# Performance work log

Measured on AMD Instinct MI355X. Metric: run time of the kernel, lower is better.

The kernel has to match this reference:

```python
import jax, jax.numpy as jnp
import numpy as np

N_A, N_B = 50000, 10000
E = 300000
IN_F, HID, BEL_OUT, INC_OUT = 256, 256, 128, 128


def _gconv(x_src, W, b, src, dst, n_src, n_dst):
    """DGL GraphConv with norm='both': D_in^{-1/2} A D_out^{-1/2} X W + b, degs clamped to >=1."""
    ones = jnp.ones(src.shape[0], x_src.dtype)
    deg_out = jnp.maximum(jax.ops.segment_sum(ones, src, num_segments=n_src), 1.0)
    deg_in = jnp.maximum(jax.ops.segment_sum(ones, dst, num_segments=n_dst), 1.0)
    h = (x_src * jax.lax.rsqrt(deg_out)[:, None]) @ W        # [n_src, out]
    agg = jax.ops.segment_sum(h[src], dst, num_segments=n_dst)  # scatter-add messages
    return agg * jax.lax.rsqrt(deg_in)[:, None] + b


def setup_inputs() -> dict:
    key = jax.random.key(0)
    ks = jax.random.split(key, 12)
    s = 1.0 / np.sqrt(IN_F)
    sh = 1.0 / np.sqrt(HID)
    return {
        "x_a": jax.random.normal(ks[0], (N_A, IN_F), jnp.float32),
        "x_b": jax.random.normal(ks[1], (N_B, IN_F), jnp.float32),
        "W1_bel": jax.random.normal(ks[2], (IN_F, HID), jnp.float32) * s,
        "b1_bel": jnp.zeros((HID,), jnp.float32),
        "W1_inc": jax.random.normal(ks[3], (IN_F, HID), jnp.float32) * s,
        "b1_inc": jnp.zeros((HID,), jnp.float32),
        "W2_bel": jax.random.normal(ks[4], (HID, BEL_OUT), jnp.float32) * sh,
        "b2_bel": jnp.zeros((BEL_OUT,), jnp.float32),
        "W2_inc": jax.random.normal(ks[5], (HID, INC_OUT), jnp.float32) * sh,
        "b2_inc": jnp.zeros((INC_OUT,), jnp.float32),
        "bel_src": jax.random.randint(ks[6], (E,), 0, N_A, jnp.int32),
        "bel_dst": jax.random.randint(ks[7], (E,), 0, N_B, jnp.int32),
        "inc_src": jax.random.randint(ks[8], (E,), 0, N_B, jnp.int32),
        "inc_dst": jax.random.randint(ks[9], (E,), 0, N_A, jnp.int32),
    }


def reference(x_a, x_b, W1_bel, b1_bel, W1_inc, b1_inc, W2_bel, b2_bel,
              W2_inc, b2_inc, bel_src, bel_dst, inc_src, inc_dst):
    n_a, n_b = x_a.shape[0], x_b.shape[0]
    # layer 1 (HeteroGraphConv, mean over a single relation per dst type = identity)
    h_b = _gconv(x_a, W1_bel, b1_bel, bel_src, bel_dst, n_a, n_b)  # 'belongs_to': A->B
    h_a = _gconv(x_b, W1_inc, b1_inc, inc_src, inc_dst, n_b, n_a)  # 'including' : B->A
    h_a = jax.nn.relu(h_a)
    h_b = jax.nn.relu(h_b)
    # layer 2
    out_b = _gconv(h_a, W2_bel, b2_bel, bel_src, bel_dst, n_a, n_b)  # [N_B, bel_out]
    out_a = _gconv(h_b, W2_inc, b2_inc, inc_src, inc_dst, n_b, n_a)  # [N_A, inc_out]
    return out_a, out_b
```

## Files before the change

### kernel.cpp

```cpp
#include <hip/hip_runtime.h>


#define NA 50000
#define NB 10000
#define NE 300000
#define GB 625
#define HB 1172
#define PB 64
#define CB 300

typedef unsigned short u16;
typedef unsigned int u32;
typedef __attribute__((ext_vector_type(8))) short short8;
typedef __attribute__((ext_vector_type(4))) float f32x4;
typedef __attribute__((ext_vector_type(2))) float f32x2;
typedef __attribute__((ext_vector_type(4))) unsigned short u16x4;

__device__ __forceinline__ float bf2f(u16 h){
  union { u32 u; float f; } x; x.u = ((u32)h) << 16; return x.f;
}
__device__ __forceinline__ u16 f2bf(float f){
  union { float f; u32 u; } x; x.f = f;
  u32 r = (x.u + 0x7FFFu + ((x.u >> 16) & 1u)) >> 16;
  return (u16)r;
}

__device__ __forceinline__ void pack_elem(int t,
    const float* __restrict__ W1b, const float* __restrict__ W1i,
    const float* __restrict__ W2b, const float* __restrict__ W2i,
    u16* __restrict__ pwh, u16* __restrict__ pwl){
  const float* W; int N; int tt;
  if (t < 65536)       { W = W1b; N = 256; tt = t; }
  else if (t < 131072) { W = W1i; N = 256; tt = t - 65536; }
  else if (t < 163840) { W = W2b; N = 128; tt = t - 131072; }
  else                 { W = W2i; N = 128; tt = t - 163840; }
  int j = tt & 7, lane = (tt >> 3) & 63, tile = tt >> 9;
  int nT = N >> 4;
  int nt = tile % nT, kt = tile / nT;
  int k = kt * 32 + ((lane >> 4) << 3) + j;
  int n = nt * 16 + (lane & 15);
  float v = W[k * N + n];
  u16 hi = f2bf(v);
  pwh[t] = hi;
  pwl[t] = f2bf(v - bf2f(hi));
}

__global__ __launch_bounds__(256) void pre_kernel(
    int* __restrict__ z, int nz, const float* __restrict__ W1i,
    u16* __restrict__ pwh, u16* __restrict__ pwl){
  int g = blockIdx.x * blockDim.x + threadIdx.x;
  int s = gridDim.x * blockDim.x;
  for (int i = g; i < nz; i += s) z[i] = 0;
  for (int t = g; t < 65536; t += s)
    pack_elem(65536 + t, nullptr, W1i, nullptr, nullptr, pwh, pwl);
}

__device__ __forceinline__ void gemm_dev(int blk, const float* __restrict__ A,
                                         const u16* __restrict__ PWH,
                                         const u16* __restrict__ PWL,
                                         const float* __restrict__ bias,
                                         const float* __restrict__ rs,
                                         float* __restrict__ Cf,
                                         u16* __restrict__ C16,
                                         int M, int nT, int wpsShift,
                                         int doRelu, int ldC, int colOff){
  int wave = blk * 4 + (threadIdx.x >> 6);
  int lane = threadIdx.x & 63;
  int strips = M >> 4;
  int strip = wave >> wpsShift;
  if (strip >= strips) return;
  int slice = wave & ((1 << wpsShift) - 1);
  int ntPer = nT >> wpsShift;
  int ntStart = slice * ntPer;
  int r16 = lane & 15, quad = lane >> 4;
  int m0 = strip << 4;
  const float* aBase = A + (size_t)(m0 + r16) * 256 + quad * 8;
  short8 ah[8], al[8];
#pragma unroll
  for (int kt = 0; kt < 8; ++kt){
    float4 p0 = *(const float4*)(aBase + kt * 32);
    float4 p1 = *(const float4*)(aBase + kt * 32 + 4);
    float v[8] = {p0.x, p0.y, p0.z, p0.w, p1.x, p1.y, p1.z, p1.w};
    short8 h, l;
#pragma unroll
    for (int j = 0; j < 8; ++j){
      u16 hb = f2bf(v[j]);
      h[j] = (short)hb;
      l[j] = (short)f2bf(v[j] - bf2f(hb));
    }
    ah[kt] = h; al[kt] = l;
  }
  float rscale[4];
#pragma unroll
  for (int r = 0; r < 4; ++r) rscale[r] = rs ? rs[m0 + quad * 4 + r] : 1.f;
  for (int nt = ntStart; nt < ntStart + ntPer; ++nt){
    f32x4 acc = {0.f, 0.f, 0.f, 0.f};
    const u16* bh = PWH + ((size_t)nt * 64 + lane) * 8;
    const u16* bl = PWL + ((size_t)nt * 64 + lane) * 8;
#pragma unroll
    for (int kt = 0; kt < 8; ++kt){
      short8 wh = *(const short8*)(bh + (size_t)kt * nT * 512);
      short8 wl = *(const short8*)(bl + (size_t)kt * nT * 512);
      acc = __builtin_amdgcn_mfma_f32_16x16x32_bf16(ah[kt], wh, acc, 0, 0, 0);
      acc = __builtin_amdgcn_mfma_f32_16x16x32_bf16(al[kt], wh, acc, 0, 0, 0);
      acc = __builtin_amdgcn_mfma_f32_16x16x32_bf16(ah[kt], wl, acc, 0, 0, 0);
    }
    int col = nt * 16 + r16;
    float bv = bias ? bias[col] : 0.f;
#pragma unroll
    for (int r = 0; r < 4; ++r){
      float v = acc[r] * rscale[r] + bv;
      if (doRelu) v = fmaxf(v, 0.f);
      size_t o = (size_t)(m0 + quad * 4 + r) * ldC + colOff + col;
      if (C16) __builtin_nontemporal_store(f2bf(v), C16 + o);
      else     __builtin_nontemporal_store(v, Cf + o);
    }
  }
}

__global__ __launch_bounds__(256) void mega_kernel(
    const float* __restrict__ xb,
    const u16* __restrict__ WH1i, const u16* __restrict__ WL1i,
    u16* __restrict__ G12,
    const int* __restrict__ bs, const int* __restrict__ bd,
    const int* __restrict__ isc, const int* __restrict__ idt,
    int* __restrict__ c_bs, int* __restrict__ c_bd,
    int* __restrict__ c_is, int* __restrict__ c_id,
    int* __restrict__ rank_bel, int* __restrict__ rank_inc,
    const float* __restrict__ W1b, const float* __restrict__ W2b,
    const float* __restrict__ W2i,
    u16* __restrict__ pwh, u16* __restrict__ pwl,
    const float* __restrict__ xa, u16* __restrict__ xa16){
  int blk = blockIdx.x;
  if (blk < GB){
    gemm_dev(blk, xb, WH1i, WL1i, nullptr, nullptr,
             nullptr, G12, NB, 16, 2, 0, 384, 0);
  } else if (blk < GB + HB){
    int g = (blk - GB) * blockDim.x + threadIdx.x;
    int s = HB * blockDim.x;
    for (int e = g; e < NE; e += s){
      atomicAdd(&c_bs[bs[e]], 1);
      rank_bel[e] = atomicAdd(&c_bd[bd[e]], 1);
      atomicAdd(&c_is[isc[e]], 1);
      rank_inc[e] = atomicAdd(&c_id[idt[e]], 1);
    }
  } else if (blk < GB + HB + PB){
    int g = (blk - GB - HB) * blockDim.x + threadIdx.x;
    int s = PB * blockDim.x;
    for (int v = g; v < 131072; v += s){
      int t = v < 65536 ? v : v + 65536;
      pack_elem(t, W1b, nullptr, W2b, W2i, pwh, pwl);
    }
  } else {
    int g = ((blk - GB - HB - PB) * blockDim.x + threadIdx.x) * 4;
    int s = CB * blockDim.x * 4;
    for (int i = g; i < NA * 256; i += s){
      float4 v = *(const float4*)(xa + i);
      u16x4 o;
      o.x = f2bf(v.x); o.y = f2bf(v.y); o.z = f2bf(v.z); o.w = f2bf(v.w);
      __builtin_nontemporal_store(o, (u16x4*)(xa16 + i));
    }
  }
}

__global__ __launch_bounds__(1024) void scan_scales_kernel(
    const int* __restrict__ c_bs, const int* __restrict__ c_bd,
    const int* __restrict__ c_is, const int* __restrict__ c_id,
    int* __restrict__ off_bel, int* __restrict__ off_inc,
    float* __restrict__ s_ob, float* __restrict__ s_ib,
    float* __restrict__ s_oi, float* __restrict__ s_ii){
  if (blockIdx.x >= 2){
    int g = (blockIdx.x - 2) * blockDim.x + threadIdx.x;
    int s = (gridDim.x - 2) * blockDim.x;
    for (int i = g; i < NA; i += s){
      int a = c_bs[i]; s_ob[i] = rsqrtf((float)(a > 1 ? a : 1));
      int b = c_id[i]; s_ii[i] = rsqrtf((float)(b > 1 ? b : 1));
      if (i < NB){
        int c = c_bd[i]; s_ib[i] = rsqrtf((float)(c > 1 ? c : 1));
        int d = c_is[i]; s_oi[i] = rsqrtf((float)(d > 1 ? d : 1));
      }
    }
    return;
  }
  const int* cnt; int* off; int n;
  if (blockIdx.x == 0){ cnt = c_bd; off = off_bel; n = NB; }
  else                { cnt = c_id; off = off_inc; n = NA; }
  __shared__ int wsum[16];
  __shared__ int carry, chunkTot;
  int tid = threadIdx.x, lane = tid & 63, wid = tid >> 6;
  if (tid == 0) carry = 0;
  __syncthreads();
  for (int base = 0; base < n; base += 4096){
    int i0 = base + tid * 4;
    int v[4];
#pragma unroll
    for (int r = 0; r < 4; ++r){ int idx = i0 + r; v[r] = (idx < n) ? cnt[idx] : 0; }
    int s = v[0] + v[1] + v[2] + v[3];
    int x = s;
#pragma unroll
    for (int d = 1; d < 64; d <<= 1){ int t = __shfl_up(x, d, 64); if (lane >= d) x += t; }
    if (lane == 63) wsum[wid] = x;
    __syncthreads();
    if (wid == 0){
      int ws = (lane < 16) ? wsum[lane] : 0;
#pragma unroll
      for (int d = 1; d < 16; d <<= 1){ int t = __shfl_up(ws, d, 64); if (lane >= d) ws += t; }
      if (lane < 16) wsum[lane] = ws;
      if (lane == 15) chunkTot = ws;
    }
    __syncthreads();
    int waveBase = (wid == 0) ? 0 : wsum[wid - 1];
    int run = carry + waveBase + (x - s);
#pragma unroll
    for (int r = 0; r < 4; ++r){ int idx = i0 + r; if (idx < n) off[idx] = run; run += v[r]; }
    __syncthreads();
    if (tid == 0) carry += chunkTot;
    __syncthreads();
  }
  if (tid == 0) off[n] = carry;
}

__global__ __launch_bounds__(256) void fill_kernel(
    const int* __restrict__ bs, const int* __restrict__ bd,
    const int* __restrict__ isc, const int* __restrict__ idt,
    const int* __restrict__ rank_bel, const int* __restrict__ rank_inc,
    const int* __restrict__ off_bel, const int* __restrict__ off_inc,
    int* __restrict__ csr_bel, int* __restrict__ csr_inc){
  int g = blockIdx.x * blockDim.x + threadIdx.x;
  int s = gridDim.x * blockDim.x;
  for (int e = g; e < NE; e += s){
    csr_bel[off_bel[bd[e]] + rank_bel[e]] = bs[e];
    csr_inc[off_inc[idt[e]] + rank_inc[e]] = isc[e];
  }
}

__global__ __launch_bounds__(256) void gemmHG_kernel(
    const float* __restrict__ Pb,
    const u16* __restrict__ WH1b, const u16* __restrict__ WL1b,
    const float* __restrict__ b1b, const float* __restrict__ s_ib,
    const u16* __restrict__ WH2i, const u16* __restrict__ WL2i,
    u16* __restrict__ G12){
  __shared__ float Hs[16][260];
  int w = threadIdx.x >> 6;
  int lane = threadIdx.x & 63;
  int r16 = lane & 15, quad = lane >> 4;
  int m0 = blockIdx.x << 4;
  const float* aBase = Pb + (size_t)(m0 + r16) * 256 + quad * 8;
  short8 ah[8], al[8];
#pragma unroll
  for (int kt = 0; kt < 8; ++kt){
    float4 p0 = *(const float4*)(aBase + kt * 32);
    float4 p1 = *(const float4*)(aBase + kt * 32 + 4);
    float v[8] = {p0.x, p0.y, p0.z, p0.w, p1.x, p1.y, p1.z, p1.w};
    short8 h, l;
#pragma unroll
    for (int j = 0; j < 8; ++j){
      u16 hb = f2bf(v[j]);
      h[j] = (short)hb;
      l[j] = (short)f2bf(v[j] - bf2f(hb));
    }
    ah[kt] = h; al[kt] = l;
  }
  float rs1[4];
#pragma unroll
  for (int r = 0; r < 4; ++r) rs1[r] = s_ib[m0 + quad * 4 + r];
  for (int nt = w * 4; nt < w * 4 + 4; ++nt){
    f32x4 acc = {0.f, 0.f, 0.f, 0.f};
    const u16* bh = WH1b + ((size_t)nt * 64 + lane) * 8;
    const u16* bl = WL1b + ((size_t)nt * 64 + lane) * 8;
#pragma unroll
    for (int kt = 0; kt < 8; ++kt){
      short8 wh = *(const short8*)(bh + (size_t)kt * 16 * 512);
      short8 wl = *(const short8*)(bl + (size_t)kt * 16 * 512);
      acc = __builtin_amdgcn_mfma_f32_16x16x32_bf16(ah[kt], wh, acc, 0, 0, 0);
      acc = __builtin_amdgcn_mfma_f32_16x16x32_bf16(al[kt], wh, acc, 0, 0, 0);
      acc = __builtin_amdgcn_mfma_f32_16x16x32_bf16(ah[kt], wl, acc, 0, 0, 0);
    }
    int col = nt * 16 + r16;
    float bv = b1b[col];
#pragma unroll
    for (int r = 0; r < 4; ++r)
      Hs[quad * 4 + r][col] = fmaxf(acc[r] * rs1[r] + bv, 0.f);
  }
  __syncthreads();
  short8 ah2[8], al2[8];
#pragma unroll
  for (int kt = 0; kt < 8; ++kt){
    float4 p0 = *(const float4*)&Hs[r16][kt * 32 + quad * 8];
    float4 p1 = *(const float4*)&Hs[r16][kt * 32 + quad * 8 + 4];
    float v[8] = {p0.x, p0.y, p0.z, p0.w, p1.x, p1.y, p1.z, p1.w};
    short8 h, l;
#pragma unroll
    for (int j = 0; j < 8; ++j){
      u16 hb = f2bf(v[j]);
      h[j] = (short)hb;
      l[j] = (short)f2bf(v[j] - bf2f(hb));
    }
    ah2[kt] = h; al2[kt] = l;
  }
  for (int nt = w * 2; nt < w * 2 + 2; ++nt){
    f32x4 acc = {0.f, 0.f, 0.f, 0.f};
    const u16* bh = WH2i + ((size_t)nt * 64 + lane) * 8;
    const u16* bl = WL2i + ((size_t)nt * 64 + lane) * 8;
#pragma unroll
    for (int kt = 0; kt < 8; ++kt){
      short8 wh = *(const short8*)(bh + (size_t)kt * 8 * 512);
      short8 wl = *(const short8*)(bl + (size_t)kt * 8 * 512);
      acc = __builtin_amdgcn_mfma_f32_16x16x32_bf16(ah2[kt], wh, acc, 0, 0, 0);
      acc = __builtin_amdgcn_mfma_f32_16x16x32_bf16(al2[kt], wh, acc, 0, 0, 0);
      acc = __builtin_amdgcn_mfma_f32_16x16x32_bf16(ah2[kt], wl, acc, 0, 0, 0);
    }
    int col = nt * 16 + r16;
#pragma unroll
    for (int r = 0; r < 4; ++r){
      u16 o = f2bf(acc[r]);
      __builtin_nontemporal_store(o, G12 + (size_t)(m0 + quad * 4 + r) * 384 + 256 + col);
    }
  }
}

__global__ __launch_bounds__(256) void agg_bel_kernel(
    const u16* __restrict__ X, const float* __restrict__ ss,
    const int* __restrict__ off, const int* __restrict__ csr,
    float* __restrict__ Pf, int nDst){
  int wave = blockIdx.x * 4 + (threadIdx.x >> 6);
  int lane = threadIdx.x & 63;
  if (wave >= nDst) return;
  int b0 = off[wave], b1 = off[wave + 1];
  int deg = b1 - b0;
  int part = lane >> 5;
  int cl = lane & 31;
  int c = cl * 8;
  float acc[8];
#pragma unroll
  for (int q = 0; q < 8; ++q) acc[q] = 0.f;
  int idx = 0; float sc = 0.f;
  if (lane < deg){
    idx = csr[b0 + lane];
    sc = ss ? ss[idx] : 1.f;
  }
  int lim = deg < 64 ? deg : 64;
  for (int u = 0; u < lim; u += 8){
    const u16* addr[4]; float w[4];
#pragma unroll
    for (int k = 0; k < 4; ++k){
      int e = u + k * 2 + part;
      int t = e < lim ? e : 0;
      int s0 = __shfl(idx, t, 64);
      float c0 = __shfl(sc, t, 64);
      w[k] = e < lim ? c0 : 0.f;
      addr[k] = X + (size_t)s0 * 256 + c;
    }
    short8 v[4];
#pragma unroll
    for (int k = 0; k < 4; ++k) v[k] = *(const short8*)addr[k];
#pragma unroll
    for (int k = 0; k < 4; ++k)
#pragma unroll
      for (int q = 0; q < 8; ++q) acc[q] += bf2f((u16)v[k][q]) * w[k];
  }
  for (int j = b0 + 64 + part; j < b1; j += 2){
    int s0 = csr[j];
    float c0 = ss ? ss[s0] : 1.f;
    short8 v0 = *(const short8*)(X + (size_t)s0 * 256 + c);
#pragma unroll
    for (int q = 0; q < 8; ++q) acc[q] += bf2f((u16)v0[q]) * c0;
  }
#pragma unroll
  for (int q = 0; q < 8; ++q) acc[q] += __shfl_xor(acc[q], 32, 64);
  if (part == 0){
    f32x4 f0 = {acc[0], acc[1], acc[2], acc[3]};
    f32x4 f1 = {acc[4], acc[5], acc[6], acc[7]};
    __builtin_nontemporal_store(f0, (f32x4*)(Pf + (size_t)wave * 256 + c));
    __builtin_nontemporal_store(f1, (f32x4*)(Pf + (size_t)wave * 256 + c + 4));
  }
}

__global__ __launch_bounds__(256) void agg_inc2_kernel(
    const u16* __restrict__ G12, const int* __restrict__ off,
    const int* __restrict__ csr, const float* __restrict__ s_oi,
    const float* __restrict__ s_ii, const float* __restrict__ s_ob,
    const float* __restrict__ b1i, const float* __restrict__ b2i,
    u16* __restrict__ Ha, float* __restrict__ outa){
  int wave = blockIdx.x * 4 + (threadIdx.x >> 6);
  int lane = threadIdx.x & 63;
  if (wave >= NA) return;
  int b0 = off[wave], b1 = off[wave + 1];
  int deg = b1 - b0;
  int c1 = lane * 4;
  int c2 = lane * 2;
  float acc[6];
#pragma unroll
  for (int q = 0; q < 6; ++q) acc[q] = 0.f;
  int idx = 0; float sc = 0.f;
  if (lane < deg){
    idx = csr[b0 + lane];
    sc = s_oi[idx];
  }
  int lim = deg < 64 ? deg : 64;
  for (int u = 0; u < lim; u += 4){
    ushort4 va[4]; ushort2 vb[4]; float w[4];
#pragma unroll
    for (int k = 0; k < 4; ++k){
      int e = u + k;
      int t = e < lim ? e : 0;
      int se = __shfl(idx, t, 64);
      float c0 = __shfl(sc, t, 64);
      w[k] = e < lim ? c0 : 0.f;
      const u16* r = G12 + (size_t)se * 384;
      va[k] = *(const ushort4*)(r + c1);
      vb[k] = *(const ushort2*)(r + 256 + c2);
    }
#pragma unroll
    for (int k = 0; k < 4; ++k){
      acc[0] += bf2f(va[k].x) * w[k];
      acc[1] += bf2f(va[k].y) * w[k];
      acc[2] += bf2f(va[k].z) * w[k];
      acc[3] += bf2f(va[k].w) * w[k];
      acc[4] += bf2f(vb[k].x) * w[k];
      acc[5] += bf2f(vb[k].y) * w[k];
    }
  }
  for (int j = b0 + 64; j < b1; ++j){
    int se = csr[j];
    float c0 = s_oi[se];
    const u16* r = G12 + (size_t)se * 384;
    ushort4 va = *(const ushort4*)(r + c1);
    ushort2 vb = *(const ushort2*)(r + 256 + c2);
    acc[0] += bf2f(va.x) * c0; acc[1] += bf2f(va.y) * c0;
    acc[2] += bf2f(va.z) * c0; acc[3] += bf2f(va.w) * c0;
    acc[4] += bf2f(vb.x) * c0; acc[5] += bf2f(vb.y) * c0;
  }
  float sii = s_ii[wave], sob = s_ob[wave];
  float4 bb1 = *(const float4*)(b1i + c1);
  f32x2 bb2 = *(const f32x2*)(b2i + c2);
  u16x4 o1;
  o1.x = f2bf(fmaxf(acc[0] * sii + bb1.x, 0.f) * sob);
  o1.y = f2bf(fmaxf(acc[1] * sii + bb1.y, 0.f) * sob);
  o1.z = f2bf(fmaxf(acc[2] * sii + bb1.z, 0.f) * sob);
  o1.w = f2bf(fmaxf(acc[3] * sii + bb1.w, 0.f) * sob);
  __builtin_nontemporal_store(o1, (u16x4*)(Ha + (size_t)wave * 256 + c1));
  f32x2 o2 = {acc[4] * sii + bb2.x, acc[5] * sii + bb2.y};
  __builtin_nontemporal_store(o2, (f32x2*)(outa + (size_t)wave * 128 + c2));
}

__global__ __launch_bounds__(256) void gemm_kernel(
    const float* __restrict__ A,
    const u16* __restrict__ PWH, const u16* __restrict__ PWL,
    const float* __restrict__ bias, const float* __restrict__ rs,
    float* __restrict__ Cf, u16* __restrict__ C16,
    int M, int nT, int wpsShift, int doRelu, int ldC, int colOff){
  gemm_dev(blockIdx.x, A, PWH, PWL, bias, rs, Cf, C16,
           M, nT, wpsShift, doRelu, ldC, colOff);
}

extern "C" void kernel_launch(void* const* d_in, const int* in_sizes, int n_in,
                              void* d_out, int out_size, void* d_ws, size_t ws_size,
                              hipStream_t stream){
  const float* x_a = (const float*)d_in[0];
  const float* x_b = (const float*)d_in[1];
  const float* W1b = (const float*)d_in[2];
  const float* b1b = (const float*)d_in[3];
  const float* W1i = (const float*)d_in[4];
  const float* b1i = (const float*)d_in[5];
  const float* W2b = (const float*)d_in[6];
  const float* b2b = (const float*)d_in[7];
  const float* W2i = (const float*)d_in[8];
  const float* b2i = (const float*)d_in[9];
  const int* bs  = (const int*)d_in[10];
  const int* bd  = (const int*)d_in[11];
  const int* isc = (const int*)d_in[12];
  const int* idt = (const int*)d_in[13];

  char* w = (char*)d_ws;
  size_t o = 0;
  auto take = [&](size_t bytes) -> void* {
    void* p = w + o; o = (o + bytes + 255) & ~(size_t)255; return p;
  };
  int* zint = (int*)take(120000 * sizeof(int));
  int* c_bs = zint, *c_bd = zint + 50000, *c_is = zint + 60000, *c_id = zint + 70000;
  int* rank_bel = (int*)take(NE * sizeof(int));
  int* rank_inc = (int*)take(NE * sizeof(int));
  int* off_bel = (int*)take((NB + 1) * sizeof(int));
  int* off_inc = (int*)take((NA + 1) * sizeof(int));
  int* csr_bel = (int*)take(NE * sizeof(int));
  int* csr_inc = (int*)take(NE * sizeof(int));
  float* s_ob = (float*)take(NA * sizeof(float));
  float* s_ib = (float*)take(NB * sizeof(float));
  float* s_oi = (float*)take(NB * sizeof(float));
  float* s_ii = (float*)take(NA * sizeof(float));
  u16* pwh = (u16*)take(196608 * sizeof(u16));
  u16* pwl = (u16*)take(196608 * sizeof(u16));
  u16* pwh1b = pwh, *pwh1i = pwh + 65536, *pwh2b = pwh + 131072, *pwh2i = pwh + 163840;
  u16* pwl1b = pwl, *pwl1i = pwl + 65536, *pwl2b = pwl + 131072, *pwl2i = pwl + 163840;
  u16* xa16 = (u16*)take((size_t)NA * 256 * sizeof(u16));
  u16* G12  = (u16*)take((size_t)NB * 384 * sizeof(u16));
  u16* H_a  = (u16*)take((size_t)NA * 256 * sizeof(u16));
  float* P_b = (float*)take((size_t)NB * 256 * sizeof(float));

  float* out_a = (float*)d_out;
  float* out_b = (float*)d_out + (size_t)NA * 128;

  pre_kernel<<<256, 256, 0, stream>>>(zint, 120000, W1i, pwh, pwl);
  mega_kernel<<<GB + HB + PB + CB, 256, 0, stream>>>(
      x_b, pwh1i, pwl1i, G12,
      bs, bd, isc, idt, c_bs, c_bd, c_is, c_id, rank_bel, rank_inc,
      W1b, W2b, W2i, pwh, pwl, x_a, xa16);
  scan_scales_kernel<<<52, 1024, 0, stream>>>(c_bs, c_bd, c_is, c_id,
                                              off_bel, off_inc,
                                              s_ob, s_ib, s_oi, s_ii);
  fill_kernel<<<1172, 256, 0, stream>>>(bs, bd, isc, idt, rank_bel, rank_inc,
                                        off_bel, off_inc, csr_bel, csr_inc);
  agg_bel_kernel<<<2500, 256, 0, stream>>>(xa16, s_ob, off_bel, csr_bel, P_b, NB);
  gemmHG_kernel<<<625, 256, 0, stream>>>(P_b, pwh1b, pwl1b, b1b, s_ib,
                                         pwh2i, pwl2i, G12);
  agg_inc2_kernel<<<12500, 256, 0, stream>>>(G12, off_inc, csr_inc, s_oi,
                                             s_ii, s_ob, b1i, b2i, H_a, out_a);
  agg_bel_kernel<<<2500, 256, 0, stream>>>(H_a, nullptr, off_bel, csr_bel, P_b, NB);
  gemm_kernel<<<625, 256, 0, stream>>>(P_b, pwh2b, pwl2b, b2b, s_ib,
                                       out_b, nullptr, NB, 8, 2, 0, 128, 0);
}
```

Before: 349.4 us.

## Fuse bel aggregation into GEMM kernels via LDS and simplify offset scan

The separate belongs_to aggregation kernels, which wrote fp32 P_b to global memory, are merged into the following GEMM kernels. Each 512-thread block gathers its 16 destination rows into LDS, then runs the split-bf16 MFMA GEMMs directly from there. This removes two launches and the global write and read of the P_b buffer. The scan kernel also drops its chunked loop with many barriers for a single pass in which each thread scans a contiguous segment. In exchange, GEMM blocks now stall on irregular gathers, and the per-thread serial segment loops give uncoalesced access.

After: 376.1 us. +7.7%, slower.

```diff
diff --git a/kernel.cpp b/kernel.cpp
--- a/kernel.cpp
+++ b/kernel.cpp
@@ -186,38 +186,27 @@
   if (blockIdx.x == 0){ cnt = c_bd; off = off_bel; n = NB; }
   else                { cnt = c_id; off = off_inc; n = NA; }
   __shared__ int wsum[16];
-  __shared__ int carry, chunkTot;
   int tid = threadIdx.x, lane = tid & 63, wid = tid >> 6;
-  if (tid == 0) carry = 0;
+  int seg = (n + 1023) >> 10;
+  int i0 = tid * seg;
+  int lim = i0 + seg; if (lim > n) lim = n;
+  int sum = 0;
+  for (int i = i0; i < lim; ++i) sum += cnt[i];
+  int x = sum;
+#pragma unroll
+  for (int d = 1; d < 64; d <<= 1){ int t = __shfl_up(x, d, 64); if (lane >= d) x += t; }
+  if (lane == 63) wsum[wid] = x;
   __syncthreads();
-  for (int base = 0; base < n; base += 4096){
-    int i0 = base + tid * 4;
-    int v[4];
-#pragma unroll
-    for (int r = 0; r < 4; ++r){ int idx = i0 + r; v[r] = (idx < n) ? cnt[idx] : 0; }
-    int s = v[0] + v[1] + v[2] + v[3];
-    int x = s;
-#pragma unroll
-    for (int d = 1; d < 64; d <<= 1){ int t = __shfl_up(x, d, 64); if (lane >= d) x += t; }
-    if (lane == 63) wsum[wid] = x;
-    __syncthreads();
-    if (wid == 0){
-      int ws = (lane < 16) ? wsum[lane] : 0;
-#pragma unroll
-      for (int d = 1; d < 16; d <<= 1){ int t = __shfl_up(ws, d, 64); if (lane >= d) ws += t; }
-      if (lane < 16) wsum[lane] = ws;
-      if (lane == 15) chunkTot = ws;
-    }
-    __syncthreads();
-    int waveBase = (wid == 0) ? 0 : wsum[wid - 1];
-    int run = carry + waveBase + (x - s);
-#pragma unroll
-    for (int r = 0; r < 4; ++r){ int idx = i0 + r; if (idx < n) off[idx] = run; run += v[r]; }
-    __syncthreads();
-    if (tid == 0) carry += chunkTot;
-    __syncthreads();
-  }
-  if (tid == 0) off[n] = carry;
+  if (wid == 0){
+    int ws = (lane < 16) ? wsum[lane] : 0;
+#pragma unroll
+    for (int d = 1; d < 16; d <<= 1){ int t = __shfl_up(ws, d, 64); if (lane >= d) ws += t; }
+    if (lane < 16) wsum[lane] = ws;
+  }
+  __syncthreads();
+  int run = (wid ? wsum[wid - 1] : 0) + (x - sum);
+  for (int i = i0; i < lim; ++i){ off[i] = run; run += cnt[i]; }
+  if (tid == 0) off[n] = wsum[15];
 }
 
 __global__ __launch_bounds__(256) void fill_kernel(
@@ -234,71 +223,129 @@
   }
 }
 
-__global__ __launch_bounds__(256) void gemmHG_kernel(
-    const float* __restrict__ Pb,
+__device__ __forceinline__ void gather_row_to_lds(
+    const u16* __restrict__ X, const float* __restrict__ ss,
+    const int* __restrict__ csr, int b0, int b1, int lane,
+    float* __restrict__ rowOut){
+  int deg = b1 - b0;
+  int part = lane >> 5;
+  int cl = lane & 31;
+  int c = cl * 8;
+  float acc[8];
+#pragma unroll
+  for (int q = 0; q < 8; ++q) acc[q] = 0.f;
+  int idx = 0; float sc = 0.f;
+  if (lane < deg){
+    idx = csr[b0 + lane];
+    sc = ss ? ss[idx] : 1.f;
+  }
+  int lim = deg < 64 ? deg : 64;
+  for (int u = 0; u < lim; u += 8){
+    const u16* addr[4]; float wv[4];
+#pragma unroll
+    for (int k = 0; k < 4; ++k){
+      int e = u + k * 2 + part;
+      int t = e < lim ? e : 0;
+      int s0 = __shfl(idx, t, 64);
+      float c0 = __shfl(sc, t, 64);
+      wv[k] = e < lim ? c0 : 0.f;
+      addr[k] = X + (size_t)s0 * 256 + c;
+    }
+    short8 v[4];
+#pragma unroll
+    for (int k = 0; k < 4; ++k) v[k] = *(const short8*)addr[k];
+#pragma unroll
+    for (int k = 0; k < 4; ++k)
+#pragma unroll
+      for (int q = 0; q < 8; ++q) acc[q] += bf2f((u16)v[k][q]) * wv[k];
+  }
+  for (int j = b0 + 64 + part; j < b1; j += 2){
+    int s0 = csr[j];
+    float c0 = ss ? ss[s0] : 1.f;
+    short8 v0 = *(const short8*)(X + (size_t)s0 * 256 + c);
+#pragma unroll
+    for (int q = 0; q < 8; ++q) acc[q] += bf2f((u16)v0[q]) * c0;
+  }
+#pragma unroll
+  for (int q = 0; q < 8; ++q) acc[q] += __shfl_xor(acc[q], 32, 64);
+  if (part == 0){
+    f32x4 f0 = {acc[0], acc[1], acc[2], acc[3]};
+    f32x4 f1 = {acc[4], acc[5], acc[6], acc[7]};
+    *(f32x4*)(rowOut + c) = f0;
+    *(f32x4*)(rowOut + c + 4) = f1;
+  }
+}
+
+__device__ __forceinline__ void encode_strip(
+    const float* __restrict__ S, int r16, int quad,
+    short8* __restrict__ ah, short8* __restrict__ al){
+#pragma unroll
+  for (int kt = 0; kt < 8; ++kt){
+    const float* p = S + (size_t)r16 * 260 + kt * 32 + quad * 8;
+    float4 p0 = *(const float4*)p;
+    float4 p1 = *(const float4*)(p + 4);
+    float v[8] = {p0.x, p0.y, p0.z, p0.w, p1.x, p1.y, p1.z, p1.w};
+    short8 h, l;
+#pragma unroll
+    for (int j = 0; j < 8; ++j){
+      u16 hb = f2bf(v[j]);
+      h[j] = (short)hb;
+      l[j] = (short)f2bf(v[j] - bf2f(hb));
+    }
+    ah[kt] = h; al[kt] = l;
+  }
+}
+
+__global__ __launch_bounds__(512) void aggGemmHG_kernel(
+    const u16* __restrict__ X, const float* __restrict__ ss,
+    const int* __restrict__ off, const int* __restrict__ csr,
     const u16* __restrict__ WH1b, const u16* __restrict__ WL1b,
     const float* __restrict__ b1b, const float* __restrict__ s_ib,
     const u16* __restrict__ WH2i, const u16* __restrict__ WL2i,
     u16* __restrict__ G12){
+  __shared__ float Ps[16][260];
   __shared__ float Hs[16][260];
   int w = threadIdx.x >> 6;
   int lane = threadIdx.x & 63;
   int r16 = lane & 15, quad = lane >> 4;
   int m0 = blockIdx.x << 4;
-  const float* aBase = Pb + (size_t)(m0 + r16) * 256 + quad * 8;
-  short8 ah[8], al[8];
-#pragma unroll
-  for (int kt = 0; kt < 8; ++kt){
-    float4 p0 = *(const float4*)(aBase + kt * 32);
-    float4 p1 = *(const float4*)(aBase + kt * 32 + 4);
-    float v[8] = {p0.x, p0.y, p0.z, p0.w, p1.x, p1.y, p1.z, p1.w};
-    short8 h, l;
-#pragma unroll
-    for (int j = 0; j < 8; ++j){
-      u16 hb = f2bf(v[j]);
-      h[j] = (short)hb;
-      l[j] = (short)f2bf(v[j] - bf2f(hb));
-    }
-    ah[kt] = h; al[kt] = l;
-  }
-  float rs1[4];
-#pragma unroll
-  for (int r = 0; r < 4; ++r) rs1[r] = s_ib[m0 + quad * 4 + r];
-  for (int nt = w * 4; nt < w * 4 + 4; ++nt){
-    f32x4 acc = {0.f, 0.f, 0.f, 0.f};
-    const u16* bh = WH1b + ((size_t)nt * 64 + lane) * 8;
-    const u16* bl = WL1b + ((size_t)nt * 64 + lane) * 8;
-#pragma unroll
-    for (int kt = 0; kt < 8; ++kt){
-      short8 wh = *(const short8*)(bh + (size_t)kt * 16 * 512);
-      short8 wl = *(const short8*)(bl + (size_t)kt * 16 * 512);
-      acc = __builtin_amdgcn_mfma_f32_16x16x32_bf16(ah[kt], wh, acc, 0, 0, 0);
-      acc = __builtin_amdgcn_mfma_f32_16x16x32_bf16(al[kt], wh, acc, 0, 0, 0);
-      acc = __builtin_amdgcn_mfma_f32_16x16x32_bf16(ah[kt], wl, acc, 0, 0, 0);
-    }
-    int col = nt * 16 + r16;
-    float bv = b1b[col];
-#pragma unroll
-    for (int r = 0; r < 4; ++r)
-      Hs[quad * 4 + r][col] = fmaxf(acc[r] * rs1[r] + bv, 0.f);
+#pragma unroll
+  for (int rr = 0; rr < 2; ++rr){
+    int row = w * 2 + rr;
+    int d = m0 + row;
+    gather_row_to_lds(X, ss, csr, off[d], off[d + 1], lane, &Ps[row][0]);
   }
   __syncthreads();
-  short8 ah2[8], al2[8];
-#pragma unroll
-  for (int kt = 0; kt < 8; ++kt){
-    float4 p0 = *(const float4*)&Hs[r16][kt * 32 + quad * 8];
-    float4 p1 = *(const float4*)&Hs[r16][kt * 32 + quad * 8 + 4];
-    float v[8] = {p0.x, p0.y, p0.z, p0.w, p1.x, p1.y, p1.z, p1.w};
-    short8 h, l;
-#pragma unroll
-    for (int j = 0; j < 8; ++j){
-      u16 hb = f2bf(v[j]);
-      h[j] = (short)hb;
-      l[j] = (short)f2bf(v[j] - bf2f(hb));
-    }
-    ah2[kt] = h; al2[kt] = l;
-  }
-  for (int nt = w * 2; nt < w * 2 + 2; ++nt){
+  {
+    short8 ah[8], al[8];
+    encode_strip(&Ps[0][0], r16, quad, ah, al);
+    float rs1[4];
+#pragma unroll
+    for (int r = 0; r < 4; ++r) rs1[r] = s_ib[m0 + quad * 4 + r];
+    for (int nt = w * 2; nt < w * 2 + 2; ++nt){
+      f32x4 acc = {0.f, 0.f, 0.f, 0.f};
+      const u16* bh = WH1b + ((size_t)nt * 64 + lane) * 8;
+      const u16* bl = WL1b + ((size_t)nt * 64 + lane) * 8;
+#pragma unroll
+      for (int kt = 0; kt < 8; ++kt){
+        short8 wh = *(const short8*)(bh + (size_t)kt * 16 * 512);
+        short8 wl = *(const short8*)(bl + (size_t)kt * 16 * 512);
+        acc = __builtin_amdgcn_mfma_f32_16x16x32_bf16(ah[kt], wh, acc, 0, 0, 0);
+        acc = __builtin_amdgcn_mfma_f32_16x16x32_bf16(al[kt], wh, acc, 0, 0, 0);
+        acc = __builtin_amdgcn_mfma_f32_16x16x32_bf16(ah[kt], wl, acc, 0, 0, 0);
+      }
+      int col = nt * 16 + r16;
+      float bv = b1b[col];
+#pragma unroll
+      for (int r = 0; r < 4; ++r)
+        Hs[quad * 4 + r][col] = fmaxf(acc[r] * rs1[r] + bv, 0.f);
+    }
+  }
+  __syncthreads();
+  {
+    short8 ah2[8], al2[8];
+    encode_strip(&Hs[0][0], r16, quad, ah2, al2);
+    int nt = w;
     f32x4 acc = {0.f, 0.f, 0.f, 0.f};
     const u16* bh = WH2i + ((size_t)nt * 64 + lane) * 8;
     const u16* bl = WL2i + ((size_t)nt * 64 + lane) * 8;
@@ -319,60 +366,47 @@
   }
 }
 
-__global__ __launch_bounds__(256) void agg_bel_kernel(
-    const u16* __restrict__ X, const float* __restrict__ ss,
+__global__ __launch_bounds__(512) void aggGemmOutB_kernel(
+    const u16* __restrict__ Ha,
     const int* __restrict__ off, const int* __restrict__ csr,
-    float* __restrict__ Pf, int nDst){
-  int wave = blockIdx.x * 4 + (threadIdx.x >> 6);
+    const u16* __restrict__ WH2b, const u16* __restrict__ WL2b,
+    const float* __restrict__ b2b, const float* __restrict__ s_ib,
+    float* __restrict__ outb){
+  __shared__ float Ps[16][260];
+  int w = threadIdx.x >> 6;
   int lane = threadIdx.x & 63;
-  if (wave >= nDst) return;
-  int b0 = off[wave], b1 = off[wave + 1];
-  int deg = b1 - b0;
-  int part = lane >> 5;
-  int cl = lane & 31;
-  int c = cl * 8;
-  float acc[8];
-#pragma unroll
-  for (int q = 0; q < 8; ++q) acc[q] = 0.f;
-  int idx = 0; float sc = 0.f;
-  if (lane < deg){
-    idx = csr[b0 + lane];
-    sc = ss ? ss[idx] : 1.f;
-  }
-  int lim = deg < 64 ? deg : 64;
-  for (int u = 0; u < lim; u += 8){
-    const u16* addr[4]; float w[4];
-#pragma unroll
-    for (int k = 0; k < 4; ++k){
-      int e = u + k * 2 + part;
-      int t = e < lim ? e : 0;
-      int s0 = __shfl(idx, t, 64);
-      float c0 = __shfl(sc, t, 64);
-      w[k] = e < lim ? c0 : 0.f;
-      addr[k] = X + (size_t)s0 * 256 + c;
-    }
-    short8 v[4];
-#pragma unroll
-    for (int k = 0; k < 4; ++k) v[k] = *(const short8*)addr[k];
-#pragma unroll
-    for (int k = 0; k < 4; ++k)
-#pragma unroll
-      for (int q = 0; q < 8; ++q) acc[q] += bf2f((u16)v[k][q]) * w[k];
-  }
-  for (int j = b0 + 64 + part; j < b1; j += 2){
-    int s0 = csr[j];
-    float c0 = ss ? ss[s0] : 1.f;
-    short8 v0 = *(const short8*)(X + (size_t)s0 * 256 + c);
-#pragma unroll
-    for (int q = 0; q < 8; ++q) acc[q] += bf2f((u16)v0[q]) * c0;
-  }
-#pragma unroll
-  for (int q = 0; q < 8; ++q) acc[q] += __shfl_xor(acc[q], 32, 64);
-  if (part == 0){
-    f32x4 f0 = {acc[0], acc[1], acc[2], acc[3]};
-    f32x4 f1 = {acc[4], acc[5], acc[6], acc[7]};
-    __builtin_nontemporal_store(f0, (f32x4*)(Pf + (size_t)wave * 256 + c));
-    __builtin_nontemporal_store(f1, (f32x4*)(Pf + (size_t)wave * 256 + c + 4));
+  int r16 = lane & 15, quad = lane >> 4;
+  int m0 = blockIdx.x << 4;
+#pragma unroll
+  for (int rr = 0; rr < 2; ++rr){
+    int row = w * 2 + rr;
+    int d = m0 + row;
+    gather_row_to_lds(Ha, nullptr, csr, off[d], off[d + 1], lane, &Ps[row][0]);
+  }
+  __syncthreads();
+  short8 ah[8], al[8];
+  encode_strip(&Ps[0][0], r16, quad, ah, al);
+  float rs1[4];
+#pragma unroll
+  for (int r = 0; r < 4; ++r) rs1[r] = s_ib[m0 + quad * 4 + r];
+  int nt = w;
+  f32x4 acc = {0.f, 0.f, 0.f, 0.f};
+  const u16* bh = WH2b + ((size_t)nt * 64 + lane) * 8;
+  const u16* bl = WL2b + ((size_t)nt * 64 + lane) * 8;
+#pragma unroll
+  for (int kt = 0; kt < 8; ++kt){
+    short8 wh = *(const short8*)(bh + (size_t)kt * 8 * 512);
+    short8 wl = *(const short8*)(bl + (size_t)kt * 8 * 512);
+    acc = __builtin_amdgcn_mfma_f32_16x16x32_bf16(ah[kt], wh, acc, 0, 0, 0);
+    acc = __builtin_amdgcn_mfma_f32_16x16x32_bf16(al[kt], wh, acc, 0, 0, 0);
+    acc = __builtin_amdgcn_mfma_f32_16x16x32_bf16(ah[kt], wl, acc, 0, 0, 0);
+  }
+  int col = nt * 16 + r16;
+  float bv = b2b[col];
+#pragma unroll
+  for (int r = 0; r < 4; ++r){
+    float v = acc[r] * rs1[r] + bv;
+    __builtin_nontemporal_store(v, outb + (size_t)(m0 + quad * 4 + r) * 128 + col);
   }
 }
 
@@ -442,16 +476,6 @@
   __builtin_nontemporal_store(o1, (u16x4*)(Ha + (size_t)wave * 256 + c1));
   f32x2 o2 = {acc[4] * sii + bb2.x, acc[5] * sii + bb2.y};
   __builtin_nontemporal_store(o2, (f32x2*)(outa + (size_t)wave * 128 + c2));
-}
-
-__global__ __launch_bounds__(256) void gemm_kernel(
-    const float* __restrict__ A,
-    const u16* __restrict__ PWH, const u16* __restrict__ PWL,
-    const float* __restrict__ bias, const float* __restrict__ rs,
-    float* __restrict__ Cf, u16* __restrict__ C16,
-    int M, int nT, int wpsShift, int doRelu, int ldC, int colOff){
-  gemm_dev(blockIdx.x, A, PWH, PWL, bias, rs, Cf, C16,
-           M, nT, wpsShift, doRelu, ldC, colOff);
 }
 
 extern "C" void kernel_launch(void* const* d_in, const int* in_sizes, int n_in,
@@ -496,7 +520,6 @@
   u16* xa16 = (u16*)take((size_t)NA * 256 * sizeof(u16));
   u16* G12  = (u16*)take((size_t)NB * 384 * sizeof(u16));
   u16* H_a  = (u16*)take((size_t)NA * 256 * sizeof(u16));
-  float* P_b = (float*)take((size_t)NB * 256 * sizeof(float));
 
   float* out_a = (float*)d_out;
   float* out_b = (float*)d_out + (size_t)NA * 128;
@@ -511,12 +534,11 @@
                                               s_ob, s_ib, s_oi, s_ii);
   fill_kernel<<<1172, 256, 0, stream>>>(bs, bd, isc, idt, rank_bel, rank_inc,
                                         off_bel, off_inc, csr_bel, csr_inc);
-  agg_bel_kernel<<<2500, 256, 0, stream>>>(xa16, s_ob, off_bel, csr_bel, P_b, NB);
-  gemmHG_kernel<<<625, 256, 0, stream>>>(P_b, pwh1b, pwl1b, b1b, s_ib,
-                                         pwh2i, pwl2i, G12);
+  aggGemmHG_kernel<<<625, 512, 0, stream>>>(xa16, s_ob, off_bel, csr_bel,
+                                            pwh1b, pwl1b, b1b, s_ib,
+                                            pwh2i, pwl2i, G12);
   agg_inc2_kernel<<<12500, 256, 0, stream>>>(G12, off_inc, csr_inc, s_oi,
                                              s_ii, s_ob, b1i, b2i, H_a, out_a);
-  agg_bel_kernel<<<2500, 256, 0, stream>>>(H_a, nullptr, off_bel, csr_bel, P_b, NB);
-  gemm_kernel<<<625, 256, 0, stream>>>(P_b, pwh2b, pwl2b, b2b, s_ib,
-                                       out_b, nullptr, NB, 8, 2, 0, 128, 0);
-}
+  aggGemmOutB_kernel<<<625, 512, 0, stream>>>(H_a, off_bel, csr_bel,
+                                              pwh2b, pwl2b, b2b, s_ib, out_b);
+}
```

## Pad degree counters to one per cache line and rewrite scan as single-pass

Applied to the files above, without the earlier changes.

Spreads each degree counter 32 ints (128 B) apart so that atomics to neighbouring nodes no longer contend on the same cache line. The zero-fill becomes vectorized nontemporal stores over a 32x larger region, and the pre kernel grid is doubled. The offset scan is rewritten as a single pass in which each thread sequentially sums a contiguous segment of strided counters, replacing the chunked multi-barrier loop. The trade-off is about 15 MB of extra zeroing traffic plus strided, uncoalesced counter reads in the scan and scale kernels. The agg_bel kernel is only moved within the file.

New measurement: 487.1 us. +39.4%, slower.

```diff
diff --git a/kernel.cpp b/kernel.cpp
--- a/kernel.cpp
+++ b/kernel.cpp
@@ -8,6 +8,7 @@
 #define HB 1172
 #define PB 64
 #define CB 300
+#define CS 32
 
 typedef unsigned short u16;
 typedef unsigned int u32;
@@ -15,6 +16,7 @@
 typedef __attribute__((ext_vector_type(4))) float f32x4;
 typedef __attribute__((ext_vector_type(2))) float f32x2;
 typedef __attribute__((ext_vector_type(4))) unsigned short u16x4;
+typedef __attribute__((ext_vector_type(4))) int i32x4;
 
 __device__ __forceinline__ float bf2f(u16 h){
   union { u32 u; float f; } x; x.u = ((u32)h) << 16; return x.f;
@@ -46,11 +48,13 @@
 }
 
 __global__ __launch_bounds__(256) void pre_kernel(
-    int* __restrict__ z, int nz, const float* __restrict__ W1i,
+    int* __restrict__ z, int nz4, const float* __restrict__ W1i,
     u16* __restrict__ pwh, u16* __restrict__ pwl){
   int g = blockIdx.x * blockDim.x + threadIdx.x;
   int s = gridDim.x * blockDim.x;
-  for (int i = g; i < nz; i += s) z[i] = 0;
+  i32x4* z4 = (i32x4*)z;
+  i32x4 zero = {0, 0, 0, 0};
+  for (int i = g; i < nz4; i += s) __builtin_nontemporal_store(zero, z4 + i);
   for (int t = g; t < 65536; t += s)
     pack_elem(65536 + t, nullptr, W1i, nullptr, nullptr, pwh, pwl);
 }
@@ -139,10 +143,10 @@
     int g = (blk - GB) * blockDim.x + threadIdx.x;
     int s = HB * blockDim.x;
     for (int e = g; e < NE; e += s){
-      atomicAdd(&c_bs[bs[e]], 1);
-      rank_bel[e] = atomicAdd(&c_bd[bd[e]], 1);
-      atomicAdd(&c_is[isc[e]], 1);
-      rank_inc[e] = atomicAdd(&c_id[idt[e]], 1);
+      atomicAdd(&c_bs[bs[e] * CS], 1);
+      rank_bel[e] = atomicAdd(&c_bd[bd[e] * CS], 1);
+      atomicAdd(&c_is[isc[e] * CS], 1);
+      rank_inc[e] = atomicAdd(&c_id[idt[e] * CS], 1);
     }
   } else if (blk < GB + HB + PB){
     int g = (blk - GB - HB) * blockDim.x + threadIdx.x;
@@ -173,11 +177,11 @@
     int g = (blockIdx.x - 2) * blockDim.x + threadIdx.x;
     int s = (gridDim.x - 2) * blockDim.x;
     for (int i = g; i < NA; i += s){
-      int a = c_bs[i]; s_ob[i] = rsqrtf((float)(a > 1 ? a : 1));
-      int b = c_id[i]; s_ii[i] = rsqrtf((float)(b > 1 ? b : 1));
+      int a = c_bs[i * CS]; s_ob[i] = rsqrtf((float)(a > 1 ? a : 1));
+      int b = c_id[i * CS]; s_ii[i] = rsqrtf((float)(b > 1 ? b : 1));
       if (i < NB){
-        int c = c_bd[i]; s_ib[i] = rsqrtf((float)(c > 1 ? c : 1));
-        int d = c_is[i]; s_oi[i] = rsqrtf((float)(d > 1 ? d : 1));
+        int c = c_bd[i * CS]; s_ib[i] = rsqrtf((float)(c > 1 ? c : 1));
+        int d = c_is[i * CS]; s_oi[i] = rsqrtf((float)(d > 1 ? d : 1));
       }
     }
     return;
@@ -186,38 +190,27 @@
   if (blockIdx.x == 0){ cnt = c_bd; off = off_bel; n = NB; }
   else                { cnt = c_id; off = off_inc; n = NA; }
   __shared__ int wsum[16];
-  __shared__ int carry, chunkTot;
   int tid = threadIdx.x, lane = tid & 63, wid = tid >> 6;
-  if (tid == 0) carry = 0;
+  int seg = (n + 1023) >> 10;
+  int i0 = tid * seg;
+  int lim = i0 + seg; if (lim > n) lim = n;
+  int sum = 0;
+  for (int i = i0; i < lim; ++i) sum += cnt[i * CS];
+  int x = sum;
+#pragma unroll
+  for (int d = 1; d < 64; d <<= 1){ int t = __shfl_up(x, d, 64); if (lane >= d) x += t; }
+  if (lane == 63) wsum[wid] = x;
   __syncthreads();
-  for (int base = 0; base < n; base += 4096){
-    int i0 = base + tid * 4;
-    int v[4];
-#pragma unroll
-    for (int r = 0; r < 4; ++r){ int idx = i0 + r; v[r] = (idx < n) ? cnt[idx] : 0; }
-    int s = v[0] + v[1] + v[2] + v[3];
-    int x = s;
-#pragma unroll
-    for (int d = 1; d < 64; d <<= 1){ int t = __shfl_up(x, d, 64); if (lane >= d) x += t; }
-    if (lane == 63) wsum[wid] = x;
-    __syncthreads();
-    if (wid == 0){
-      int ws = (lane < 16) ? wsum[lane] : 0;
-#pragma unroll
-      for (int d = 1; d < 16; d <<= 1){ int t = __shfl_up(ws, d, 64); if (lane >= d) ws += t; }
-      if (lane < 16) wsum[lane] = ws;
-      if (lane == 15) chunkTot = ws;
-    }
-    __syncthreads();
-    int waveBase = (wid == 0) ? 0 : wsum[wid - 1];
-    int run = carry + waveBase + (x - s);
-#pragma unroll
-    for (int r = 0; r < 4; ++r){ int idx = i0 + r; if (idx < n) off[idx] = run; run += v[r]; }
-    __syncthreads();
-    if (tid == 0) carry += chunkTot;
-    __syncthreads();
-  }
-  if (tid == 0) off[n] = carry;
+  if (wid == 0){
+    int ws = (lane < 16) ? wsum[lane] : 0;
+#pragma unroll
+    for (int d = 1; d < 16; d <<= 1){ int t = __shfl_up(ws, d, 64); if (lane >= d) ws += t; }
+    if (lane < 16) wsum[lane] = ws;
+  }
+  __syncthreads();
+  int run = (wid ? wsum[wid - 1] : 0) + (x - sum);
+  for (int i = i0; i < lim; ++i){ off[i] = run; run += cnt[i * CS]; }
+  if (tid == 0) off[n] = wsum[15];
 }
 
 __global__ __launch_bounds__(256) void fill_kernel(
@@ -231,6 +224,63 @@
   for (int e = g; e < NE; e += s){
     csr_bel[off_bel[bd[e]] + rank_bel[e]] = bs[e];
     csr_inc[off_inc[idt[e]] + rank_inc[e]] = isc[e];
+  }
+}
+
+__global__ __launch_bounds__(256) void agg_bel_kernel(
+    const u16* __restrict__ X, const float* __restrict__ ss,
+    const int* __restrict__ off, const int* __restrict__ csr,
+    float* __restrict__ Pf, int nDst){
+  int wave = blockIdx.x * 4 + (threadIdx.x >> 6);
+  int lane = threadIdx.x & 63;
+  if (wave >= nDst) return;
+  int b0 = off[wave], b1 = off[wave + 1];
+  int deg = b1 - b0;
+  int part = lane >> 5;
+  int cl = lane & 31;
+  int c = cl * 8;
+  float acc[8];
+#pragma unroll
+  for (int q = 0; q < 8; ++q) acc[q] = 0.f;
+  int idx = 0; float sc = 0.f;
+  if (lane < deg){
+    idx = csr[b0 + lane];
+    sc = ss ? ss[idx] : 1.f;
+  }
+  int lim = deg < 64 ? deg : 64;
+  for (int u = 0; u < lim; u += 8){
+    const u16* addr[4]; float w[4];
+#pragma unroll
+    for (int k = 0; k < 4; ++k){
+      int e = u + k * 2 + part;
+      int t = e < lim ? e : 0;
+      int s0 = __shfl(idx, t, 64);
+      float c0 = __shfl(sc, t, 64);
+      w[k] = e < lim ? c0 : 0.f;
+      addr[k] = X + (size_t)s0 * 256 + c;
+    }
+    short8 v[4];
+#pragma unroll
+    for (int k = 0; k < 4; ++k) v[k] = *(const short8*)addr[k];
+#pragma unroll
+    for (int k = 0; k < 4; ++k)
+#pragma unroll
+      for (int q = 0; q < 8; ++q) acc[q] += bf2f((u16)v[k][q]) * w[k];
+  }
+  for (int j = b0 + 64 + part; j < b1; j += 2){
+    int s0 = csr[j];
+    float c0 = ss ? ss[s0] : 1.f;
+    short8 v0 = *(const short8*)(X + (size_t)s0 * 256 + c);
+#pragma unroll
+    for (int q = 0; q < 8; ++q) acc[q] += bf2f((u16)v0[q]) * c0;
+  }
+#pragma unroll
+  for (int q = 0; q < 8; ++q) acc[q] += __shfl_xor(acc[q], 32, 64);
+  if (part == 0){
+    f32x4 f0 = {acc[0], acc[1], acc[2], acc[3]};
+    f32x4 f1 = {acc[4], acc[5], acc[6], acc[7]};
+    __builtin_nontemporal_store(f0, (f32x4*)(Pf + (size_t)wave * 256 + c));
+    __builtin_nontemporal_store(f1, (f32x4*)(Pf + (size_t)wave * 256 + c + 4));
   }
 }
 
@@ -316,63 +366,6 @@
       u16 o = f2bf(acc[r]);
       __builtin_nontemporal_store(o, G12 + (size_t)(m0 + quad * 4 + r) * 384 + 256 + col);
     }
-  }
-}
-
-__global__ __launch_bounds__(256) void agg_bel_kernel(
-    const u16* __restrict__ X, const float* __restrict__ ss,
-    const int* __restrict__ off, const int* __restrict__ csr,
-    float* __restrict__ Pf, int nDst){
-  int wave = blockIdx.x * 4 + (threadIdx.x >> 6);
-  int lane = threadIdx.x & 63;
-  if (wave >= nDst) return;
-  int b0 = off[wave], b1 = off[wave + 1];
-  int deg = b1 - b0;
-  int part = lane >> 5;
-  int cl = lane & 31;
-  int c = cl * 8;
-  float acc[8];
-#pragma unroll
-  for (int q = 0; q < 8; ++q) acc[q] = 0.f;
-  int idx = 0; float sc = 0.f;
-  if (lane < deg){
-    idx = csr[b0 + lane];
-    sc = ss ? ss[idx] : 1.f;
-  }
-  int lim = deg < 64 ? deg : 64;
-  for (int u = 0; u < lim; u += 8){
-    const u16* addr[4]; float w[4];
-#pragma unroll
-    for (int k = 0; k < 4; ++k){
-      int e = u + k * 2 + part;
-      int t = e < lim ? e : 0;
-      int s0 = __shfl(idx, t, 64);
-      float c0 = __shfl(sc, t, 64);
-      w[k] = e < lim ? c0 : 0.f;
-      addr[k] = X + (size_t)s0 * 256 + c;
-    }
-    short8 v[4];
-#pragma unroll
-    for (int k = 0; k < 4; ++k) v[k] = *(const short8*)addr[k];
-#pragma unroll
-    for (int k = 0; k < 4; ++k)
-#pragma unroll
-      for (int q = 0; q < 8; ++q) acc[q] += bf2f((u16)v[k][q]) * w[k];
-  }
-  for (int j = b0 + 64 + part; j < b1; j += 2){
-    int s0 = csr[j];
-    float c0 = ss ? ss[s0] : 1.f;
-    short8 v0 = *(const short8*)(X + (size_t)s0 * 256 + c);
-#pragma unroll
-    for (int q = 0; q < 8; ++q) acc[q] += bf2f((u16)v0[q]) * c0;
-  }
-#pragma unroll
-  for (int q = 0; q < 8; ++q) acc[q] += __shfl_xor(acc[q], 32, 64);
-  if (part == 0){
-    f32x4 f0 = {acc[0], acc[1], acc[2], acc[3]};
-    f32x4 f1 = {acc[4], acc[5], acc[6], acc[7]};
-    __builtin_nontemporal_store(f0, (f32x4*)(Pf + (size_t)wave * 256 + c));
-    __builtin_nontemporal_store(f1, (f32x4*)(Pf + (size_t)wave * 256 + c + 4));
   }
 }
 
@@ -477,8 +470,11 @@
   auto take = [&](size_t bytes) -> void* {
     void* p = w + o; o = (o + bytes + 255) & ~(size_t)255; return p;
   };
-  int* zint = (int*)take(120000 * sizeof(int));
-  int* c_bs = zint, *c_bd = zint + 50000, *c_is = zint + 60000, *c_id = zint + 70000;
+  int* zint = (int*)take((size_t)120000 * CS * sizeof(int));
+  int* c_bs = zint;
+  int* c_bd = zint + (size_t)50000 * CS;
+  int* c_is = zint + (size_t)60000 * CS;
+  int* c_id = zint + (size_t)70000 * CS;
   int* rank_bel = (int*)take(NE * sizeof(int));
   int* rank_inc = (int*)take(NE * sizeof(int));
   int* off_bel = (int*)take((NB + 1) * sizeof(int));
@@ -501,7 +497,7 @@
   float* out_a = (float*)d_out;
   float* out_b = (float*)d_out + (size_t)NA * 128;
 
-  pre_kernel<<<256, 256, 0, stream>>>(zint, 120000, W1i, pwh, pwl);
+  pre_kernel<<<512, 256, 0, stream>>>(zint, 120000 * CS / 4, W1i, pwh, pwl);
   mega_kernel<<<GB + HB + PB + CB, 256, 0, stream>>>(
       x_b, pwh1i, pwl1i, G12,
       bs, bd, isc, idt, c_bs, c_bd, c_is, c_id, rank_bel, rank_inc,
```
